# Kernel tuning notes

Hardware: AMD Instinct MI355X
Metric: run time of the kernel (lower is better)

The kernel has to match this reference:

```python
import jax, jax.numpy as jnp
import numpy as np

QMIN, QMAX = -128, 127  # signed int8 range


def setup_inputs() -> dict:
    key = jax.random.key(0)
    k_x, k_w, k_b = jax.random.split(key, 3)
    N, C_in, H, W = 32, 128, 56, 56
    C_out, kH, kW = 256, 3, 3
    # int8-valued tensors carried as int32 (jax-friendly); values in [-128, 127]
    x = jax.random.randint(k_x, (N, C_in, H, W), 0, 256, dtype=jnp.int32) - 128
    weight = jax.random.randint(k_w, (C_out, C_in, kH, kW), 0, 256, dtype=jnp.int32) - 128
    # int32 bias, already quantized with scale s_in * s_w
    bias = jax.random.randint(k_b, (C_out,), -(2 ** 14), 2 ** 14, dtype=jnp.int32)
    return {
        "x": x,
        "weight": weight,
        "bias": bias,
        "input_scale": jnp.float32(0.02),
        "weight_scale": jnp.float32(0.005),
        "output_scale": jnp.float32(0.05),
        "input_zero_point": jnp.int32(-5),
        "output_zero_point": jnp.int32(3),
    }


def reference(x, weight, bias, input_scale, weight_scale, output_scale,
              input_zero_point, output_zero_point):
    # Dequant-style integer conv: shift input by its zero point (weights are
    # symmetric, zero point 0), accumulate in fp32 (stands in for int32 acc).
    x_f = (x - input_zero_point).astype(jnp.float32)
    w_f = weight.astype(jnp.float32)
    acc = jax.lax.conv_general_dilated(
        x_f, w_f,
        window_strides=(1, 1),
        padding=((1, 1), (1, 1)),
        dimension_numbers=("NCHW", "OIHW", "NCHW"),
    )
    acc = acc + bias.astype(jnp.float32)[None, :, None, None]
    # Requantize: scale fusion + output zero point, round, clamp to int8.
    requant_scale = input_scale * weight_scale / output_scale
    y = acc * requant_scale + output_zero_point.astype(jnp.float32)
    y_q = jnp.clip(jnp.round(y), QMIN, QMAX).astype(jnp.int8)
    return y_q
```

## Files before the change

kernel.cpp:

```cpp
#include <hip/hip_runtime.h>
#include <stdint.h>


#define NB 32
#define CI 128
#define HH 56
#define WW 56
#define CO 256
#define SPA (HH * WW)
#define HP 58
#define WP 64
#define XP2_BYTES (NB * HP * WP * CI)
#define BP_BYTES (9 * 2 * 4 * CO * 16)
#define ABUF (4 * 8192)

typedef int v4i __attribute__((ext_vector_type(4)));

__global__ __launch_bounds__(256) void prep_kernel(
    const int* __restrict__ x, const int* __restrict__ wgt,
    const int* __restrict__ bias, const int* __restrict__ zpi,
    int8_t* __restrict__ xp2, int8_t* __restrict__ bp, int* __restrict__ BG)
{
    __shared__ int sm[1824];
    const int tid = threadIdx.x, bid = blockIdx.x;
    const int zp = *zpi;
    const int zp4 = (zp & 255) * 0x01010101;

    if (bid < HH * NB) {
        const int n = bid / HH, h = bid % HH;
        #pragma unroll
        for (int it = 0; it < 7; ++it) {
            int j = tid + it * 256;
            int ci = j / 14, w4 = j - ci * 14;
            const v4i v = *(const v4i*)(x + ((n * CI + ci) * HH + h) * WW + w4 * 4);
            sm[w4 * 130 + ci] = (v.x & 255) | ((v.y & 255) << 8) |
                                ((v.z & 255) << 16) | (v.w << 24);
        }
        __syncthreads();
        int* od = (int*)xp2 + (n * HP + h + 1) * (WP * CI / 4);
        #pragma unroll
        for (int it = 0; it < 8; ++it) {
            int j = tid + it * 256;
            int widx = j >> 5, ci4 = j & 31;
            int val = zp4;
            if (widx >= 1 && widx <= WW) {
                int w = widx - 1;
                int base = (w >> 2) * 130 + ci4 * 4;
                int sh = (w & 3) * 8;
                val = ((sm[base] >> sh) & 0xff) | (((sm[base+1] >> sh) & 0xff) << 8) |
                      (((sm[base+2] >> sh) & 0xff) << 16) | ((sm[base+3] >> sh) << 24);
            }
            od[j ^ ((widx & 7) << 2)] = val;
        }
    } else if (bid < HH * NB + 2 * NB) {
        const int z = bid - HH * NB;
        const int n = z >> 1, hidx = (z & 1) ? (HP - 1) : 0;
        int* od = (int*)xp2 + (n * HP + hidx) * (WP * CI / 4);
        #pragma unroll
        for (int it = 0; it < 8; ++it) od[tid + it * 256] = zp4;
    } else {
        const int co = bid - (HH * NB + 2 * NB);
        for (int j = tid; j < 1152; j += 256) sm[j] = wgt[co * 1152 + j];
        __syncthreads();
        for (int j = tid; j < 288; j += 256) {
            int j4 = j & 3, q = (j >> 2) & 3, c64 = (j >> 4) & 1, t = j >> 5;
            int ci = c64 * 64 + q * 16 + j4 * 4;
            int b0 = sm[(ci + 0) * 9 + t] & 255, b1 = sm[(ci + 1) * 9 + t] & 255;
            int b2 = sm[(ci + 2) * 9 + t] & 255, b3 = sm[(ci + 3) * 9 + t];
            ((int*)bp)[((t * 2 + c64) * 4 + q) * 1024 + co * 4 + j4] =
                b0 | (b1 << 8) | (b2 << 16) | (b3 << 24);
        }
        if (tid < 9) {
            int s = 0;
            for (int ci = 0; ci < CI; ++ci) s += sm[ci * 9 + tid];
            sm[1152 + tid] = s;
        }
        __syncthreads();
        if (tid == 0) {
            int s9 = 0;
            for (int t = 0; t < 9; ++t) s9 += sm[1152 + t];
            BG[co] = bias[co] - zp * s9;
        }
    }
}

__global__ __launch_bounds__(256, 2) void qconv_mfma(
    const int8_t* __restrict__ xp2, const int8_t* __restrict__ bp,
    const int* __restrict__ BG,
    const float* __restrict__ si, const float* __restrict__ sw,
    const float* __restrict__ so, const int* __restrict__ zpo,
    int* __restrict__ out)
{
    const int tid  = threadIdx.x, lane = tid & 63, wid = tid >> 6;
    const int quad = lane >> 4, lo16 = lane & 15;
    const int bid  = blockIdx.x;
    const int xcd  = bid & 7, i = bid >> 3;
    const int n    = xcd * 4 + (i & 3);
    const int cb   = (i >> 2) & 1;
    const int sA   = i >> 3;
    const int ntiles = (i < 32) ? 4 : 3;
    const int cw   = cb * 128 + wid * 32;

    __shared__ __attribute__((aligned(16))) int8_t Asm[2][ABUF];

    const int8_t* src0 = xp2 + (((size_t)n * HP + 2 * sA) << 13);
    #pragma unroll
    for (int k = 0; k < 8; ++k) {
        const int u = wid + 4 * k;
        __builtin_amdgcn_global_load_lds(
            (const __attribute__((address_space(1))) void*)(src0 + (u << 10) + lane * 16),
            (__attribute__((address_space(3))) void*)(&Asm[0][u << 10]), 16, 0, 0);
    }

    int bgv[2];
    #pragma unroll
    for (int ct = 0; ct < 2; ++ct) bgv[ct] = BG[cw + ct * 16 + lo16];
    const float rs = (*si) * (*sw) / (*so);
    const float zo = (float)(*zpo);

    int boff[7], sw3[7];
    #pragma unroll
    for (int mt = 0; mt < 7; ++mt) {
        const int ml = mt * 16 + lo16;
        const int srow = ml / 56, scol = ml - srow * 56;
        boff[mt] = srow * 8192 + scol * 128 + quad * 16;
        int s0 = ((scol + 0) & 7) << 4, s1 = ((scol + 1) & 7) << 4,
            s2 = ((scol + 2) & 7) << 4;
        sw3[mt] = s0 | (s1 << 8) | (s2 << 16);
    }

    const int8_t* bwav = bp + ((size_t)quad << 12) + ((cw + lo16) << 4);

    int* optr0 = out + ((size_t)n * CO + cw + lo16) * SPA + quad * 4;
    int* optr1 = optr0 + 16 * SPA;

    __syncthreads();

    #define BLOAD(tp) {                                                        \
        const int8_t* bb = bwav + ((tp) * 8 << 12);                            \
        asm volatile("" : "+v"(bb));                                           \
        bt[tp][0] = *(const v4i*)(bb);                                         \
        bt[tp][1] = *(const v4i*)(bb + 256);                                   \
        bt[tp][2] = *(const v4i*)(bb + 16384);                                 \
        bt[tp][3] = *(const v4i*)(bb + 16384 + 256);                           \
    }

    #pragma unroll 1
    for (int j = 0; j < ntiles; ++j) {
        const int s = sA + 8 * j;
        const int8_t* curA = Asm[j & 1];

        v4i bt[9][4];
        BLOAD(0); BLOAD(1);

        if (j + 1 < ntiles) {
            const int8_t* srcn = xp2 + (((size_t)n * HP + 2 * (s + 8)) << 13);
            int8_t* dst = (int8_t*)Asm[(j & 1) ^ 1];
            #pragma unroll
            for (int k = 0; k < 8; ++k) {
                const int u = wid + 4 * k;
                __builtin_amdgcn_global_load_lds(
                    (const __attribute__((address_space(1))) void*)(srcn + (u << 10) + lane * 16),
                    (__attribute__((address_space(3))) void*)(dst + (u << 10)), 16, 0, 0);
            }
        }
        __builtin_amdgcn_sched_barrier(0);

        v4i acc[7][2];
        #pragma unroll
        for (int mt = 0; mt < 7; ++mt) {
            acc[mt][0] = (v4i){0, 0, 0, 0};
            acc[mt][1] = (v4i){0, 0, 0, 0};
        }

        __builtin_amdgcn_s_setprio(1);
        #pragma unroll
        for (int tp = 0; tp < 9; ++tp) {
            if (tp + 2 <= 8) BLOAD(tp + 2);
            const int dr = tp / 3, dc = tp % 3;
            #pragma unroll
            for (int mt = 0; mt < 7; ++mt) {
                const int off  = boff[mt] + dr * 8192 + dc * 128;
                const int phys = off ^ ((sw3[mt] >> (8 * dc)) & 0x70);
                v4i a0 = *(const v4i*)(curA + phys);
                v4i a1 = *(const v4i*)(curA + (phys ^ 64));
                acc[mt][0] = __builtin_amdgcn_mfma_i32_16x16x64_i8(a0, bt[tp][0], acc[mt][0], 0, 0, 0);
                acc[mt][1] = __builtin_amdgcn_mfma_i32_16x16x64_i8(a0, bt[tp][1], acc[mt][1], 0, 0, 0);
                acc[mt][0] = __builtin_amdgcn_mfma_i32_16x16x64_i8(a1, bt[tp][2], acc[mt][0], 0, 0, 0);
                acc[mt][1] = __builtin_amdgcn_mfma_i32_16x16x64_i8(a1, bt[tp][3], acc[mt][1], 0, 0, 0);
            }
        }
        __builtin_amdgcn_s_setprio(0);

        const int m0 = s * 112;
        #pragma unroll
        for (int mt = 0; mt < 7; ++mt) {
            v4i v0, v1;
            #pragma unroll
            for (int i4 = 0; i4 < 4; ++i4) {
                float y0 = rintf((float)(acc[mt][0][i4] + bgv[0]) * rs + zo);
                float y1 = rintf((float)(acc[mt][1][i4] + bgv[1]) * rs + zo);
                v0[i4] = (int)fminf(fmaxf(y0, -128.f), 127.f);
                v1[i4] = (int)fminf(fmaxf(y1, -128.f), 127.f);
            }
            *(v4i*)(optr0 + m0 + mt * 16) = v0;
            *(v4i*)(optr1 + m0 + mt * 16) = v1;
        }

        if (j + 1 < ntiles) {
            __builtin_amdgcn_sched_barrier(0);
            asm volatile("s_waitcnt vmcnt(14)" ::: "memory");
            __builtin_amdgcn_s_barrier();
            __builtin_amdgcn_sched_barrier(0);
        }
    }
    #undef BLOAD
}

extern "C" void kernel_launch(void* const* d_in, const int* in_sizes, int n_in,
                              void* d_out, int out_size, void* d_ws, size_t ws_size,
                              hipStream_t stream) {
    const int*   x    = (const int*)d_in[0];
    const int*   wgt  = (const int*)d_in[1];
    const int*   bias = (const int*)d_in[2];
    const float* si   = (const float*)d_in[3];
    const float* sw   = (const float*)d_in[4];
    const float* so   = (const float*)d_in[5];
    const int*   zpi  = (const int*)d_in[6];
    const int*   zpo  = (const int*)d_in[7];
    int* out = (int*)d_out;

    int8_t* xp2 = (int8_t*)d_ws;
    int8_t* bp  = xp2 + XP2_BYTES;
    int*    bg  = (int*)(bp + BP_BYTES);

    prep_kernel<<<HH * NB + 2 * NB + CO, 256, 0, stream>>>(x, wgt, bias, zpi, xp2, bp, bg);
    qconv_mfma<<<512, 256, 0, stream>>>(xp2, bp, bg, si, sw, so, zpo, out);
}
```

Before: 187.6 us.

## Replace persistent double-buffered tile loop with one tile per block grid

The conv kernel no longer has each block loop over 3-4 spatial tiles with double-buffered LDS prefetch. It now launches 1792 blocks, each computing a single spatial tile with a single LDS buffer, and drops the launch_bounds occupancy hint. This removes the explicit software pipelining and load imbalance across the 512 persistent blocks and relies on hardware scheduling of more, smaller blocks to hide latency. In exchange, each block pays its own load and startup cost, and the B-fragment loads are no longer amortized across tiles.

```diff
diff --git a/kernel.cpp b/kernel.cpp
--- a/kernel.cpp
+++ b/kernel.cpp
@@ -84,7 +84,7 @@
     }
 }
 
-__global__ __launch_bounds__(256, 2) void qconv_mfma(
+__global__ __launch_bounds__(256) void qconv_mfma(
     const int8_t* __restrict__ xp2, const int8_t* __restrict__ bp,
     const int* __restrict__ BG,
     const float* __restrict__ si, const float* __restrict__ sw,
@@ -94,22 +94,21 @@
     const int tid  = threadIdx.x, lane = tid & 63, wid = tid >> 6;
     const int quad = lane >> 4, lo16 = lane & 15;
     const int bid  = blockIdx.x;
-    const int xcd  = bid & 7, i = bid >> 3;
-    const int n    = xcd * 4 + (i & 3);
-    const int cb   = (i >> 2) & 1;
-    const int sA   = i >> 3;
-    const int ntiles = (i < 32) ? 4 : 3;
+    const int xcd  = bid & 7, idx = bid >> 3;
+    const int n    = xcd * 4 + (idx & 3);
+    const int cb   = (idx >> 2) & 1;
+    const int s2   = idx >> 3;
     const int cw   = cb * 128 + wid * 32;
 
-    __shared__ __attribute__((aligned(16))) int8_t Asm[2][ABUF];
-
-    const int8_t* src0 = xp2 + (((size_t)n * HP + 2 * sA) << 13);
+    __shared__ __attribute__((aligned(16))) int8_t Asm[ABUF];
+
+    const int8_t* src0 = xp2 + (((size_t)n * HP + 2 * s2) << 13);
     #pragma unroll
     for (int k = 0; k < 8; ++k) {
         const int u = wid + 4 * k;
         __builtin_amdgcn_global_load_lds(
             (const __attribute__((address_space(1))) void*)(src0 + (u << 10) + lane * 16),
-            (__attribute__((address_space(3))) void*)(&Asm[0][u << 10]), 16, 0, 0);
+            (__attribute__((address_space(3))) void*)(&Asm[u << 10]), 16, 0, 0);
     }
 
     int bgv[2];
@@ -125,16 +124,14 @@
         const int srow = ml / 56, scol = ml - srow * 56;
         boff[mt] = srow * 8192 + scol * 128 + quad * 16;
         int s0 = ((scol + 0) & 7) << 4, s1 = ((scol + 1) & 7) << 4,
-            s2 = ((scol + 2) & 7) << 4;
-        sw3[mt] = s0 | (s1 << 8) | (s2 << 16);
+            s2x = ((scol + 2) & 7) << 4;
+        sw3[mt] = s0 | (s1 << 8) | (s2x << 16);
     }
 
     const int8_t* bwav = bp + ((size_t)quad << 12) + ((cw + lo16) << 4);
 
     int* optr0 = out + ((size_t)n * CO + cw + lo16) * SPA + quad * 4;
     int* optr1 = optr0 + 16 * SPA;
-
-    __syncthreads();
 
     #define BLOAD(tp) {                                                        \
         const int8_t* bb = bwav + ((tp) * 8 << 12);                            \
@@ -145,76 +142,52 @@
         bt[tp][3] = *(const v4i*)(bb + 16384 + 256);                           \
     }
 
-    #pragma unroll 1
-    for (int j = 0; j < ntiles; ++j) {
-        const int s = sA + 8 * j;
-        const int8_t* curA = Asm[j & 1];
-
-        v4i bt[9][4];
-        BLOAD(0); BLOAD(1);
-
-        if (j + 1 < ntiles) {
-            const int8_t* srcn = xp2 + (((size_t)n * HP + 2 * (s + 8)) << 13);
-            int8_t* dst = (int8_t*)Asm[(j & 1) ^ 1];
-            #pragma unroll
-            for (int k = 0; k < 8; ++k) {
-                const int u = wid + 4 * k;
-                __builtin_amdgcn_global_load_lds(
-                    (const __attribute__((address_space(1))) void*)(srcn + (u << 10) + lane * 16),
-                    (__attribute__((address_space(3))) void*)(dst + (u << 10)), 16, 0, 0);
-            }
-        }
-        __builtin_amdgcn_sched_barrier(0);
-
-        v4i acc[7][2];
+    v4i bt[9][4];
+    BLOAD(0); BLOAD(1);
+
+    v4i acc[7][2];
+    #pragma unroll
+    for (int mt = 0; mt < 7; ++mt) {
+        acc[mt][0] = (v4i){0, 0, 0, 0};
+        acc[mt][1] = (v4i){0, 0, 0, 0};
+    }
+
+    __syncthreads();
+
+    __builtin_amdgcn_s_setprio(1);
+    #pragma unroll
+    for (int tp = 0; tp < 9; ++tp) {
+        if (tp + 2 <= 8) BLOAD(tp + 2);
+        const int dr = tp / 3, dc = tp % 3;
         #pragma unroll
         for (int mt = 0; mt < 7; ++mt) {
-            acc[mt][0] = (v4i){0, 0, 0, 0};
-            acc[mt][1] = (v4i){0, 0, 0, 0};
-        }
-
-        __builtin_amdgcn_s_setprio(1);
-        #pragma unroll
-        for (int tp = 0; tp < 9; ++tp) {
-            if (tp + 2 <= 8) BLOAD(tp + 2);
-            const int dr = tp / 3, dc = tp % 3;
-            #pragma unroll
-            for (int mt = 0; mt < 7; ++mt) {
-                const int off  = boff[mt] + dr * 8192 + dc * 128;
-                const int phys = off ^ ((sw3[mt] >> (8 * dc)) & 0x70);
-                v4i a0 = *(const v4i*)(curA + phys);
-                v4i a1 = *(const v4i*)(curA + (phys ^ 64));
-                acc[mt][0] = __builtin_amdgcn_mfma_i32_16x16x64_i8(a0, bt[tp][0], acc[mt][0], 0, 0, 0);
-                acc[mt][1] = __builtin_amdgcn_mfma_i32_16x16x64_i8(a0, bt[tp][1], acc[mt][1], 0, 0, 0);
-                acc[mt][0] = __builtin_amdgcn_mfma_i32_16x16x64_i8(a1, bt[tp][2], acc[mt][0], 0, 0, 0);
-                acc[mt][1] = __builtin_amdgcn_mfma_i32_16x16x64_i8(a1, bt[tp][3], acc[mt][1], 0, 0, 0);
-            }
-        }
-        __builtin_amdgcn_s_setprio(0);
-
-        const int m0 = s * 112;
-        #pragma unroll
-        for (int mt = 0; mt < 7; ++mt) {
-            v4i v0, v1;
-            #pragma unroll
-            for (int i4 = 0; i4 < 4; ++i4) {
-                float y0 = rintf((float)(acc[mt][0][i4] + bgv[0]) * rs + zo);
-                float y1 = rintf((float)(acc[mt][1][i4] + bgv[1]) * rs + zo);
-                v0[i4] = (int)fminf(fmaxf(y0, -128.f), 127.f);
-                v1[i4] = (int)fminf(fmaxf(y1, -128.f), 127.f);
-            }
-            *(v4i*)(optr0 + m0 + mt * 16) = v0;
-            *(v4i*)(optr1 + m0 + mt * 16) = v1;
-        }
-
-        if (j + 1 < ntiles) {
-            __builtin_amdgcn_sched_barrier(0);
-            asm volatile("s_waitcnt vmcnt(14)" ::: "memory");
-            __builtin_amdgcn_s_barrier();
-            __builtin_amdgcn_sched_barrier(0);
-        }
-    }
+            const int off  = boff[mt] + dr * 8192 + dc * 128;
+            const int phys = off ^ ((sw3[mt] >> (8 * dc)) & 0x70);
+            v4i a0 = *(const v4i*)(Asm + phys);
+            v4i a1 = *(const v4i*)(Asm + (phys ^ 64));
+            acc[mt][0] = __builtin_amdgcn_mfma_i32_16x16x64_i8(a0, bt[tp][0], acc[mt][0], 0, 0, 0);
+            acc[mt][1] = __builtin_amdgcn_mfma_i32_16x16x64_i8(a0, bt[tp][1], acc[mt][1], 0, 0, 0);
+            acc[mt][0] = __builtin_amdgcn_mfma_i32_16x16x64_i8(a1, bt[tp][2], acc[mt][0], 0, 0, 0);
+            acc[mt][1] = __builtin_amdgcn_mfma_i32_16x16x64_i8(a1, bt[tp][3], acc[mt][1], 0, 0, 0);
+        }
+    }
+    __builtin_amdgcn_s_setprio(0);
     #undef BLOAD
+
+    const int m0 = s2 * 112;
+    #pragma unroll
+    for (int mt = 0; mt < 7; ++mt) {
+        v4i v0, v1;
+        #pragma unroll
+        for (int i4 = 0; i4 < 4; ++i4) {
+            float y0 = rintf((float)(acc[mt][0][i4] + bgv[0]) * rs + zo);
+            float y1 = rintf((float)(acc[mt][1][i4] + bgv[1]) * rs + zo);
+            v0[i4] = (int)fminf(fmaxf(y0, -128.f), 127.f);
+            v1[i4] = (int)fminf(fmaxf(y1, -128.f), 127.f);
+        }
+        *(v4i*)(optr0 + m0 + mt * 16) = v0;
+        *(v4i*)(optr1 + m0 + mt * 16) = v1;
+    }
 }
 
 extern "C" void kernel_launch(void* const* d_in, const int* in_sizes, int n_in,
@@ -235,5 +208,5 @@
     int*    bg  = (int*)(bp + BP_BYTES);
 
     prep_kernel<<<HH * NB + 2 * NB + CO, 256, 0, stream>>>(x, wgt, bias, zpi, xp2, bp, bg);
-    qconv_mfma<<<512, 256, 0, stream>>>(xp2, bp, bg, si, sw, so, zpo, out);
+    qconv_mfma<<<1792, 256, 0, stream>>>(xp2, bp, bg, si, sw, so, zpo, out);
 }
```

Result: no change. 190.1 us (+1.3%).
